# Kernel optimization log

Hardware: AMD Instinct MI355X
Metric: run time of the kernel (lower is better)

The kernel has to match this reference:

```python
import jax, jax.numpy as jnp
import numpy as np

BS, L, NIMG, D, H, DH, V, NL = 16, 256, 256, 512, 8, 256, 1000, 6


def _softmax_one(x):
    # softmax with +1 in denominator (post max-shift, literal +1 as in source)
    m = jnp.max(x, axis=-1, keepdims=True)
    e = jnp.exp(x - m)
    return e / (1.0 + jnp.sum(e, axis=-1, keepdims=True))


def _ln(x, g, b):
    mu = jnp.mean(x, axis=-1, keepdims=True)
    var = jnp.var(x, axis=-1, keepdims=True)
    return (x - mu) * jax.lax.rsqrt(var + 1e-5) * g + b


def _mha(xq, xkv, wq, b_q, wk, b_k, wv, b_v, wo, b_o, mask):
    b, nq, _ = xq.shape
    nk = xkv.shape[1]
    q = (xq @ wq + b_q).reshape(b, nq, H, DH).transpose(0, 2, 1, 3)
    k = (xkv @ wk + b_k).reshape(b, nk, H, DH).transpose(0, 2, 1, 3)
    v = (xkv @ wv + b_v).reshape(b, nk, H, DH).transpose(0, 2, 1, 3)
    s = jnp.einsum('bhqd,bhkd->bhqk', q, k) / jnp.sqrt(jnp.float32(DH))
    if mask is not None:
        s = s + mask[:, None]  # (b,1,nq,nk) additive mask
    o = jnp.einsum('bhqk,bhkd->bhqd', _softmax_one(s), v)
    return o.transpose(0, 2, 1, 3).reshape(b, nq, H * DH) @ wo + b_o


def _forward(program, pro_adj, img_features, embed, W_in, b_in, ln1_g, ln1_b, ln2_g, ln2_b,
             Wq, bq, Wk, bk, Wv, bv, Wo, bo, f_W1, f_b1, f_W2, f_b2,
             cWq, cbq, cWk, cbk, cWv, cbv, cWo, cbo):
    mask = (1.0 - pro_adj.astype(jnp.float32)) * -1e6
    bs, length = program.shape[:2]
    x = embed[program].reshape(bs, length, -1) @ W_in + b_in  # (bs, L, D)
    for i in range(NL):
        # self-attn transformer layer (pre-LN, residual)
        h = _ln(x, ln1_g[i], ln1_b[i])
        x = x + _mha(h, h, Wq[i], bq[i], Wk[i], bk[i], Wv[i], bv[i], Wo[i], bo[i], mask)
        h2 = _ln(x, ln2_g[i], ln2_b[i])
        x = x + (jax.nn.gelu(h2 @ f_W1[i] + f_b1[i], approximate=False) @ f_W2[i] + f_b2[i])
        # cross-modal attention to image features, residual add
        x = x + _mha(x, img_features, cWq[i], cbq[i], cWk[i], cbk[i], cWv[i], cbv[i], cWo[i], cbo[i], None)
    return x


def setup_inputs() -> dict:
    key = jax.random.key(0)
    ks = jax.random.split(key, 16)
    def n(k, shape):
        return jax.random.normal(k, shape, jnp.float32) * 0.02
    program = jax.random.randint(ks[0], (BS, L, 8), 0, V, dtype=jnp.int32)
    pro_adj = jax.random.randint(ks[1], (BS, L, L), 0, 2, dtype=jnp.int32)
    img_features = jax.random.normal(ks[2], (BS, NIMG, D), jnp.float32)
    embed = n(ks[3], (V, 300)).at[0].set(0.0)  # padding_idx=0
    return dict(
        program=program, pro_adj=pro_adj, img_features=img_features, embed=embed,
        W_in=n(ks[4], (8 * 300, D)), b_in=jnp.zeros((D,), jnp.float32),
        ln1_g=jnp.ones((NL, D), jnp.float32), ln1_b=jnp.zeros((NL, D), jnp.float32),
        ln2_g=jnp.ones((NL, D), jnp.float32), ln2_b=jnp.zeros((NL, D), jnp.float32),
        Wq=n(ks[5], (NL, D, H * DH)), bq=jnp.zeros((NL, H * DH), jnp.float32),
        Wk=n(ks[6], (NL, D, H * DH)), bk=jnp.zeros((NL, H * DH), jnp.float32),
        Wv=n(ks[7], (NL, D, H * DH)), bv=jnp.zeros((NL, H * DH), jnp.float32),
        Wo=n(ks[8], (NL, H * DH, D)), bo=jnp.zeros((NL, D), jnp.float32),
        f_W1=n(ks[9], (NL, D, D)), f_b1=jnp.zeros((NL, D), jnp.float32),
        f_W2=n(ks[10], (NL, D, D)), f_b2=jnp.zeros((NL, D), jnp.float32),
        cWq=n(ks[11], (NL, D, H * DH)), cbq=jnp.zeros((NL, H * DH), jnp.float32),
        cWk=n(ks[12], (NL, D, H * DH)), cbk=jnp.zeros((NL, H * DH), jnp.float32),
        cWv=n(ks[13], (NL, D, H * DH)), cbv=jnp.zeros((NL, H * DH), jnp.float32),
        cWo=n(ks[14], (NL, H * DH, D)), cbo=jnp.zeros((NL, D), jnp.float32),
    )


def reference(program, pro_adj, img_features, embed, W_in, b_in, ln1_g, ln1_b, ln2_g, ln2_b,
              Wq, bq, Wk, bk, Wv, bv, Wo, bo, f_W1, f_b1, f_W2, f_b2,
              cWq, cbq, cWk, cbk, cWv, cbv, cWo, cbo):
    return _forward(program, pro_adj, img_features, embed, W_in, b_in, ln1_g, ln1_b, ln2_g, ln2_b,
                    Wq, bq, Wk, bk, Wv, bv, Wo, bo, f_W1, f_b1, f_W2, f_b2,
                    cWq, cbq, cWk, cbk, cWv, cbv, cWo, cbo)
```

## Files before the change

kernel.cpp:

```cpp
#include <hip/hip_runtime.h>
#include <hip/hip_bf16.h>

typedef __attribute__((ext_vector_type(8))) short short8;
typedef __attribute__((ext_vector_type(4))) float f32x4;
typedef unsigned short u16;

__device__ __forceinline__ u16 f2b(float f) {
    unsigned int u = __builtin_bit_cast(unsigned int, f);
    u = u + 0x7fffu + ((u >> 16) & 1u);
    return (u16)(u >> 16);
}

#define EPI_F32      0
#define EPI_RESID_XB 3
#define EPI_GELU     4
#define EPI_KV       7
#define EPI_ATOMIC   9

template<int BM, int BN, int BK, int EPI>
__global__ __launch_bounds__(256, 2) void gemm_bf16(
    const u16* __restrict__ A, long aStride, int lda,
    const u16* __restrict__ B, long bStride, int ldb,
    int M, int N, int K,
    const float* __restrict__ bias0, const float* __restrict__ bias1,
    int biasStride,
    const float* __restrict__ Rsd,
    float* __restrict__ outF, u16* __restrict__ outB,
    u16* __restrict__ outV, long outStride, int ldc)
{
    constexpr int WCOLS = BN / 64;
    constexpr int WROWS = 4 / WCOLS;
    constexpr int WM = BM / WROWS;
    constexpr int MF = WM / 16;
    constexpr int NF = 4;
    constexpr int GR = BK / 8;
    constexpr int AUNITS = BM * GR;
    constexpr int UPT = (BM + BN) * GR / 256;
    constexpr int BUFE = (BM + BN) * BK;

    __shared__ __align__(16) u16 smem[2 * BUFE];

    const int tid = threadIdx.x;
    const int wave = tid >> 6, lane = tid & 63;
    const int wm = wave / WCOLS, wn = wave % WCOLS;

    const int nwg = gridDim.x * gridDim.y;
    const int bl = blockIdx.y * gridDim.x + blockIdx.x;
    const int wsw = (bl & 7) * (nwg >> 3) + (bl >> 3);
    const int bxs = wsw % gridDim.x, bys = wsw / gridDim.x;

    const int tm = bys * BM, tn = bxs * BN;
    const int bz = blockIdx.z;

    const size_t aOff = (size_t)bz * (size_t)aStride;
    const size_t bOff = (size_t)bz * (size_t)bStride;

    const int lr = lane & 15, kg = lane >> 4;

    auto stage = [&](int buf, int k0) {
#pragma unroll
        for (int i = 0; i < UPT; i++) {
            int u = tid + i * 256;
            u16* dst = smem + buf * BUFE + u * 8;
            bool isA = u < AUNITS;
            int v = isA ? u : u - AUNITS;
            int row, kloc;
            if constexpr (BK == 64) {
                row = v >> 3;
                int hh = (v >> 2) & 1, g = v & 3;
                kloc = ((hh ^ (row & 1)) << 5) + ((g ^ ((row >> 1) & 3)) << 3);
            } else {
                row = v >> 2;
                int g = v & 3;
                kloc = (g ^ ((row >> 1) & 3)) << 3;
            }
            const u16* src = isA
                ? A + aOff + (size_t)(tm + row) * lda + k0 + kloc
                : B + bOff + (size_t)(tn + row) * ldb + k0 + kloc;
            __builtin_amdgcn_global_load_lds(src, dst, 16, 0, 0);
        }
    };

    auto ldsOff = [&](int row, int kk) -> int {
        if constexpr (BK == 64)
            return row * 64 + (((kk ^ (row & 1)) * 4 + (kg ^ ((row >> 1) & 3))) * 8);
        else
            return row * 32 + ((kg ^ ((row >> 1) & 3)) * 8);
    };

    f32x4 acc[MF][NF];
#pragma unroll
    for (int m = 0; m < MF; m++)
#pragma unroll
        for (int n = 0; n < NF; n++) acc[m][n] = (f32x4)(0.f);

    const int NT = K / BK;
    stage(0, 0);
    __syncthreads();

    for (int t = 0; t < NT; t++) {
        const int cur = t & 1;
        if (t + 1 < NT) stage(cur ^ 1, (t + 1) * BK);

        const u16* As = smem + cur * BUFE;
        const u16* Bs = As + BM * BK;
#pragma unroll
        for (int kk = 0; kk < BK / 32; kk++) {
            short8 af[MF], bfr[NF];
#pragma unroll
            for (int m = 0; m < MF; m++) {
                int row = wm * WM + m * 16 + lr;
                af[m] = *(const short8*)&As[ldsOff(row, kk)];
            }
#pragma unroll
            for (int n = 0; n < NF; n++) {
                int row = wn * 64 + n * 16 + lr;
                bfr[n] = *(const short8*)&Bs[ldsOff(row, kk)];
            }
#pragma unroll
            for (int m = 0; m < MF; m++)
#pragma unroll
                for (int n = 0; n < NF; n++)
                    acc[m][n] = __builtin_amdgcn_mfma_f32_16x16x32_bf16(
                        af[m], bfr[n], acc[m][n], 0, 0, 0);
        }
        __syncthreads();
    }

    if constexpr (EPI == EPI_KV) {
        if (tn < 2048) {
#pragma unroll
            for (int m = 0; m < MF; m++)
#pragma unroll
                for (int n = 0; n < NF; n++)
#pragma unroll
                    for (int e = 0; e < 4; e++) {
                        int r = tm + wm * WM + m * 16 + kg * 4 + e;
                        int c = tn + wn * 64 + n * 16 + lr;
                        float t = acc[m][n][e] + bias0[bz * biasStride + c];
                        outB[(size_t)bz * outStride + (size_t)r * 2048 + c] = f2b(t);
                    }
        } else {
            const int ccb = tn - 2048;
            const int bidx = tm >> 8;
            const int hh = ccb >> 8;
            u16* vls = smem;
#pragma unroll
            for (int m = 0; m < MF; m++)
#pragma unroll
                for (int n = 0; n < NF; n++)
#pragma unroll
                    for (int e = 0; e < 4; e++) {
                        int rl = wm * WM + m * 16 + kg * 4 + e;
                        int cl = wn * 64 + n * 16 + lr;
                        float t = acc[m][n][e] + bias1[bz * biasStride + ccb + cl];
                        vls[cl * 136 + rl] = f2b(t);
                    }
            __syncthreads();
            const int dloc = tid >> 1;
            const int thalf = (tid & 1) * 64;
            const int dglob = (ccb & 255) + dloc;
            u16* dst = outV + (size_t)bz * outStride +
                       (size_t)(bidx * 8 + hh) * 65536 +
                       (size_t)dglob * 256 + (tm & 255) + thalf;
            const u16* srcl = vls + dloc * 136 + thalf;
#pragma unroll
            for (int k = 0; k < 8; k++)
                *(uint4*)(dst + k * 8) = *(const uint4*)(srcl + k * 8);
        }
        return;
    }

#pragma unroll
    for (int m = 0; m < MF; m++) {
#pragma unroll
        for (int n = 0; n < NF; n++) {
#pragma unroll
            for (int e = 0; e < 4; e++) {
                int r = tm + wm * WM + m * 16 + (lane >> 4) * 4 + e;
                int c = tn + wn * 64 + n * 16 + (lane & 15);
                float v = acc[m][n][e];
                if constexpr (EPI == EPI_F32) {
                    outF[(size_t)r * ldc + c] = v + bias0[c];
                } else if constexpr (EPI == EPI_RESID_XB) {
                    float t = v + bias0[c] + Rsd[(size_t)r * ldc + c];
                    outF[(size_t)r * ldc + c] = t;
                    outB[(size_t)r * ldc + c] = f2b(t);
                } else if constexpr (EPI == EPI_GELU) {
                    float t = v + bias0[c];
                    t = 0.5f * t * (1.f + erff(t * 0.70710678118654752f));
                    outB[(size_t)r * ldc + c] = f2b(t);
                } else if constexpr (EPI == EPI_ATOMIC) {
                    float t = v;
                    if (bz == 0) t += bias0[c];
                    atomicAdd(&outF[(size_t)r * ldc + c], t);
                }
            }
        }
    }
}

template<bool MASKED>
__global__ __launch_bounds__(256, 2) void attn_kernel(
    const u16* __restrict__ Aq, const u16* __restrict__ WqT,
    const float* __restrict__ bq,
    const u16* __restrict__ K, const u16* __restrict__ Vt,
    const int* __restrict__ adj, u16* __restrict__ O)
{
    __shared__ __align__(16) u16 Ps[64 * 256];
    __shared__ __align__(16) u16 Ks[2 * 256 * 32];
    __shared__ __align__(16) u16 Aql[2 * 64 * 32];
    __shared__ float red1[64 * 4];
    __shared__ float red2[64 * 4];

    const int tid = threadIdx.x;
    const int w = tid >> 6, lane = tid & 63;
    const int lr = lane & 15, kg = lane >> 4;

    const int nwg = gridDim.x * gridDim.y;
    const int bl = blockIdx.y * gridDim.x + blockIdx.x;
    const int wsw = (bl & 7) * (nwg >> 3) + (bl >> 3);
    const int qt = wsw % gridDim.x, bh = wsw / gridDim.x;

    const int b = bh >> 3, h = bh & 7;
    const size_t qkBase = (size_t)b * 256 * 2048 + h * 256;

    auto stageA0 = [&](int buf, int k0) {
        int u = tid;
        int row = u >> 2, g = u & 3;
        int gs = g ^ ((row >> 1) & 3);
        const u16* src = Aq + (size_t)(b * 256 + qt * 64 + row) * 512 + k0 + gs * 8;
        __builtin_amdgcn_global_load_lds(src, Aql + buf * 2048 + u * 8, 16, 0, 0);
    };
    auto stageB0 = [&](int buf, int k0) {
#pragma unroll
        for (int i = 0; i < 4; i++) {
            int u = tid + i * 256;
            int row = u >> 2, g = u & 3;
            int gs = g ^ ((row >> 1) & 3);
            const u16* src = WqT + (size_t)(h * 256 + row) * 512 + k0 + gs * 8;
            __builtin_amdgcn_global_load_lds(src, Ks + buf * 8192 + u * 8, 16, 0, 0);
        }
    };
    auto stageK = [&](int buf, int dk) {
#pragma unroll
        for (int i = 0; i < 4; i++) {
            int u = tid + i * 256;
            int row = u >> 2, g = u & 3;
            int gs = g ^ ((row >> 1) & 3);
            const u16* src = K + qkBase + (size_t)row * 2048 + dk * 32 + gs * 8;
            __builtin_amdgcn_global_load_lds(src, Ks + buf * 8192 + u * 8, 16, 0, 0);
        }
    };
    auto stageV = [&](int buf, int kt) {
#pragma unroll
        for (int i = 0; i < 4; i++) {
            int u = tid + i * 256;
            int row = u >> 2, g = u & 3;
            int gs = g ^ ((row >> 1) & 3);
            const u16* src = Vt + (size_t)bh * 65536 + (size_t)row * 256 + kt * 32 + gs * 8;
            __builtin_amdgcn_global_load_lds(src, Ks + buf * 8192 + u * 8, 16, 0, 0);
        }
    };

    {
        f32x4 qacc[4][4];
#pragma unroll
        for (int m = 0; m < 4; m++)
#pragma unroll
            for (int n = 0; n < 4; n++) qacc[m][n] = (f32x4)(0.f);

        stageA0(0, 0);
        stageB0(0, 0);
        __syncthreads();
        for (int t = 0; t < 16; t++) {
            const int cur = t & 1;
            if (t < 15) { stageA0(cur ^ 1, (t + 1) * 32); stageB0(cur ^ 1, (t + 1) * 32); }
            short8 af[4], bfr[4];
#pragma unroll
            for (int m = 0; m < 4; m++) {
                int row = m * 16 + lr;
                af[m] = *(const short8*)&Aql[cur * 2048 + row * 32 + ((kg ^ ((row >> 1) & 3)) * 8)];
            }
#pragma unroll
            for (int n = 0; n < 4; n++) {
                int row = w * 64 + n * 16 + lr;
                bfr[n] = *(const short8*)&Ks[cur * 8192 + row * 32 + ((kg ^ ((row >> 1) & 3)) * 8)];
            }
            __builtin_amdgcn_s_setprio(1);
#pragma unroll
            for (int m = 0; m < 4; m++)
#pragma unroll
                for (int n = 0; n < 4; n++)
                    qacc[m][n] = __builtin_amdgcn_mfma_f32_16x16x32_bf16(
                        af[m], bfr[n], qacc[m][n], 0, 0, 0);
            __builtin_amdgcn_s_setprio(0);
            __syncthreads();
        }
#pragma unroll
        for (int m = 0; m < 4; m++)
#pragma unroll
            for (int n = 0; n < 4; n++)
#pragma unroll
                for (int e = 0; e < 4; e++) {
                    int q = m * 16 + kg * 4 + e;
                    int d = w * 64 + n * 16 + lr;
                    float t = qacc[m][n][e] + bq[h * 256 + d];
                    Ps[q * 256 + (((d >> 3) ^ (q & 7)) * 8) + (d & 7)] = f2b(t);
                }
    }
    __syncthreads();

    f32x4 sacc[4][4];
#pragma unroll
    for (int m = 0; m < 4; m++)
#pragma unroll
        for (int n = 0; n < 4; n++) sacc[m][n] = (f32x4)(0.f);

    stageK(0, 0);
    __syncthreads();
    for (int dk = 0; dk < 8; dk++) {
        const int cur = dk & 1;
        if (dk < 7) stageK(cur ^ 1, dk + 1);
        short8 af[4], bfr[4];
#pragma unroll
        for (int m = 0; m < 4; m++) {
            int row = m * 16 + lr;
            af[m] = *(const short8*)&Ps[row * 256 + (((dk * 4 + kg) ^ (row & 7)) * 8)];
        }
#pragma unroll
        for (int n = 0; n < 4; n++) {
            int row = w * 64 + n * 16 + lr;
            bfr[n] = *(const short8*)&Ks[cur * 8192 + row * 32 + ((kg ^ ((row >> 1) & 3)) * 8)];
        }
        __builtin_amdgcn_s_setprio(1);
#pragma unroll
        for (int m = 0; m < 4; m++)
#pragma unroll
            for (int n = 0; n < 4; n++)
                sacc[m][n] = __builtin_amdgcn_mfma_f32_16x16x32_bf16(
                    af[m], bfr[n], sacc[m][n], 0, 0, 0);
        __builtin_amdgcn_s_setprio(0);
        __syncthreads();
    }

    stageV(0, 0);

#pragma unroll
    for (int m = 0; m < 4; m++)
#pragma unroll
        for (int n = 0; n < 4; n++)
#pragma unroll
            for (int e = 0; e < 4; e++) {
                float t = sacc[m][n][e] * 0.0625f;
                if (MASKED) {
                    int q = qt * 64 + m * 16 + kg * 4 + e;
                    int k = w * 64 + n * 16 + lr;
                    int a_ = adj[((size_t)b * 256 + q) * 256 + k];
                    t += (1.f - (float)a_) * -1.0e6f;
                }
                sacc[m][n][e] = t;
            }

    float mx[4][4];
#pragma unroll
    for (int m = 0; m < 4; m++)
#pragma unroll
        for (int e = 0; e < 4; e++) {
            float v = sacc[m][0][e];
#pragma unroll
            for (int n = 1; n < 4; n++) v = fmaxf(v, sacc[m][n][e]);
#pragma unroll
            for (int off = 1; off < 16; off <<= 1) v = fmaxf(v, __shfl_xor(v, off));
            mx[m][e] = v;
        }
    if (lr == 0) {
#pragma unroll
        for (int m = 0; m < 4; m++)
#pragma unroll
            for (int e = 0; e < 4; e++)
                red1[(m * 16 + kg * 4 + e) * 4 + w] = mx[m][e];
    }
    __syncthreads();

    float inv[4][4];
    float sum[4][4];
#pragma unroll
    for (int m = 0; m < 4; m++)
#pragma unroll
        for (int e = 0; e < 4; e++) {
            int r = m * 16 + kg * 4 + e;
            float gm = fmaxf(fmaxf(red1[r * 4 + 0], red1[r * 4 + 1]),
                             fmaxf(red1[r * 4 + 2], red1[r * 4 + 3]));
            float s = 0.f;
#pragma unroll
            for (int n = 0; n < 4; n++) {
                float ev = __expf(sacc[m][n][e] - gm);
                sacc[m][n][e] = ev;
                s += ev;
            }
            sum[m][e] = s;
        }
#pragma unroll
    for (int m = 0; m < 4; m++)
#pragma unroll
        for (int e = 0; e < 4; e++) {
            float s = sum[m][e];
#pragma unroll
            for (int off = 1; off < 16; off <<= 1) s += __shfl_xor(s, off);
            sum[m][e] = s;
        }
    if (lr == 0) {
#pragma unroll
        for (int m = 0; m < 4; m++)
#pragma unroll
            for (int e = 0; e < 4; e++)
                red2[(m * 16 + kg * 4 + e) * 4 + w] = sum[m][e];
    }
    __syncthreads();
#pragma unroll
    for (int m = 0; m < 4; m++)
#pragma unroll
        for (int e = 0; e < 4; e++) {
            int r = m * 16 + kg * 4 + e;
            float gs = red2[r * 4 + 0] + red2[r * 4 + 1] +
                       red2[r * 4 + 2] + red2[r * 4 + 3];
            inv[m][e] = 1.f / (1.f + gs);
        }

#pragma unroll
    for (int m = 0; m < 4; m++)
#pragma unroll
        for (int n = 0; n < 4; n++)
#pragma unroll
            for (int e = 0; e < 4; e++) {
                int q = m * 16 + kg * 4 + e;
                int k = w * 64 + n * 16 + lr;
                float pv = sacc[m][n][e] * inv[m][e];
                Ps[q * 256 + (((k >> 3) ^ (q & 7)) * 8) + (k & 7)] = f2b(pv);
            }
    __syncthreads();

    f32x4 oacc[4][4];
#pragma unroll
    for (int m = 0; m < 4; m++)
#pragma unroll
        for (int n = 0; n < 4; n++) oacc[m][n] = (f32x4)(0.f);

    for (int kt = 0; kt < 8; kt++) {
        const int cur = kt & 1;
        if (kt < 7) stageV(cur ^ 1, kt + 1);
        short8 af[4], bfr[4];
#pragma unroll
        for (int m = 0; m < 4; m++) {
            int q = m * 16 + lr;
            af[m] = *(const short8*)&Ps[q * 256 + (((kt * 4 + kg) ^ (q & 7)) * 8)];
        }
#pragma unroll
        for (int n = 0; n < 4; n++) {
            int row = w * 64 + n * 16 + lr;
            bfr[n] = *(const short8*)&Ks[cur * 8192 + row * 32 + ((kg ^ ((row >> 1) & 3)) * 8)];
        }
        __builtin_amdgcn_s_setprio(1);
#pragma unroll
        for (int m = 0; m < 4; m++)
#pragma unroll
            for (int n = 0; n < 4; n++)
                oacc[m][n] = __builtin_amdgcn_mfma_f32_16x16x32_bf16(
                    af[m], bfr[n], oacc[m][n], 0, 0, 0);
        __builtin_amdgcn_s_setprio(0);
        __syncthreads();
    }

#pragma unroll
    for (int m = 0; m < 4; m++)
#pragma unroll
        for (int n = 0; n < 4; n++)
#pragma unroll
            for (int e = 0; e < 4; e++) {
                int q = qt * 64 + m * 16 + kg * 4 + e;
                int d = w * 64 + n * 16 + lr;
                O[(size_t)(b * 256 + q) * 2048 + h * 256 + d] = f2b(oacc[m][n][e]);
            }
}

__global__ __launch_bounds__(256) void transpose_kernel(
    const float* p0, const float* p1, const float* p2,
    const float* p3, const float* p4, const float* p5,
    int nsrc, long srcLayerStride, int R, int C,
    u16* __restrict__ out, long dstMatStride, long dstLayerStride)
{
    const int mat = blockIdx.z % nsrc, layer = blockIdx.z / nsrc;
    const float* W;
    switch (mat) {
    default: W = p0; break;
    case 1: W = p1; break;
    case 2: W = p2; break;
    case 3: W = p3; break;
    case 4: W = p4; break;
    case 5: W = p5; break;
    }
    W += (size_t)layer * srcLayerStride;
    u16* o = out + (size_t)layer * dstLayerStride + (size_t)mat * dstMatStride;
    __shared__ float t[64][65];
    const int tid = threadIdx.x;
    const int rBase = blockIdx.y * 64, cBase = blockIdx.x * 64;
#pragma unroll
    for (int i = 0; i < 4; i++) {
        int idx = tid + i * 256;
        int rr = idx >> 4, cc4 = (idx & 15) * 4;
        if (rBase + rr < R) {
            float4 v = *(const float4*)&W[(size_t)(rBase + rr) * C + cBase + cc4];
            t[rr][cc4] = v.x; t[rr][cc4 + 1] = v.y;
            t[rr][cc4 + 2] = v.z; t[rr][cc4 + 3] = v.w;
        }
    }
    __syncthreads();
#pragma unroll
    for (int i = 0; i < 4; i++) {
        int idx = tid + i * 256;
        int cc = idx >> 4, rr4 = (idx & 15) * 4;
        if (rBase + rr4 < R) {
            uint2 pk;
            pk.x = (unsigned)f2b(t[rr4][cc]) | ((unsigned)f2b(t[rr4 + 1][cc]) << 16);
            pk.y = (unsigned)f2b(t[rr4 + 2][cc]) | ((unsigned)f2b(t[rr4 + 3][cc]) << 16);
            *(uint2*)&o[(size_t)(cBase + cc) * R + rBase + rr4] = pk;
        }
    }
}

__global__ __launch_bounds__(256) void ln_kernel(
    const float* __restrict__ X, const float* __restrict__ g,
    const float* __restrict__ b, u16* __restrict__ Y)
{
    const int wave = threadIdx.x >> 6, lane = threadIdx.x & 63;
    const size_t row = (size_t)blockIdx.x * 4 + wave;
    const float* xr = X + row * 512;
    float4 v0 = *reinterpret_cast<const float4*>(xr + lane * 8);
    float4 v1 = *reinterpret_cast<const float4*>(xr + lane * 8 + 4);
    float s = v0.x + v0.y + v0.z + v0.w + v1.x + v1.y + v1.z + v1.w;
    float ss = v0.x * v0.x + v0.y * v0.y + v0.z * v0.z + v0.w * v0.w +
               v1.x * v1.x + v1.y * v1.y + v1.z * v1.z + v1.w * v1.w;
#pragma unroll
    for (int off = 32; off; off >>= 1) {
        s += __shfl_xor(s, off);
        ss += __shfl_xor(ss, off);
    }
    float mu = s * (1.0f / 512.0f);
    float var = ss * (1.0f / 512.0f) - mu * mu;
    float rs = rsqrtf(var + 1e-5f);
    float4 g0 = *reinterpret_cast<const float4*>(g + lane * 8);
    float4 g1 = *reinterpret_cast<const float4*>(g + lane * 8 + 4);
    float4 b0 = *reinterpret_cast<const float4*>(b + lane * 8);
    float4 b1 = *reinterpret_cast<const float4*>(b + lane * 8 + 4);
    float o0 = (v0.x - mu) * rs * g0.x + b0.x;
    float o1 = (v0.y - mu) * rs * g0.y + b0.y;
    float o2 = (v0.z - mu) * rs * g0.z + b0.z;
    float o3 = (v0.w - mu) * rs * g0.w + b0.w;
    float o4 = (v1.x - mu) * rs * g1.x + b1.x;
    float o5 = (v1.y - mu) * rs * g1.y + b1.y;
    float o6 = (v1.z - mu) * rs * g1.z + b1.z;
    float o7 = (v1.w - mu) * rs * g1.w + b1.w;
    uint4 pk;
    pk.x = (unsigned)f2b(o0) | ((unsigned)f2b(o1) << 16);
    pk.y = (unsigned)f2b(o2) | ((unsigned)f2b(o3) << 16);
    pk.z = (unsigned)f2b(o4) | ((unsigned)f2b(o5) << 16);
    pk.w = (unsigned)f2b(o6) | ((unsigned)f2b(o7) << 16);
    *reinterpret_cast<uint4*>(Y + row * 512 + lane * 8) = pk;
}

__global__ __launch_bounds__(256) void gather_kernel(
    const int* __restrict__ program, const float* __restrict__ embed,
    unsigned* __restrict__ Ag2, int total2)
{
    int idx = blockIdx.x * 256 + threadIdx.x;
    if (idx >= total2) return;
    int t = idx / 1200;
    int rem = idx - t * 1200;
    int j = rem / 150;
    int e2 = rem - j * 150;
    int tok = program[t * 8 + j];
    float2 v = *reinterpret_cast<const float2*>(&embed[(size_t)tok * 300 + e2 * 2]);
    Ag2[idx] = (unsigned)f2b(v.x) | ((unsigned)f2b(v.y) << 16);
}

__global__ __launch_bounds__(256) void cvt_kernel(
    const float* __restrict__ in, u16* __restrict__ out, int n4)
{
    int i = blockIdx.x * 256 + threadIdx.x;
    if (i >= n4) return;
    float4 v = reinterpret_cast<const float4*>(in)[i];
    uint2 pk;
    pk.x = (unsigned)f2b(v.x) | ((unsigned)f2b(v.y) << 16);
    pk.y = (unsigned)f2b(v.z) | ((unsigned)f2b(v.w) << 16);
    reinterpret_cast<uint2*>(out)[i] = pk;
}


extern "C" void kernel_launch(void* const* d_in, const int* in_sizes, int n_in,
                              void* d_out, int out_size, void* d_ws, size_t ws_size,
                              hipStream_t stream)
{
    const int*   program = (const int*)d_in[0];
    const int*   adj     = (const int*)d_in[1];
    const float* img     = (const float*)d_in[2];
    const float* embed   = (const float*)d_in[3];
    const float* W_in    = (const float*)d_in[4];
    const float* b_in    = (const float*)d_in[5];
    const float* ln1_g   = (const float*)d_in[6];
    const float* ln1_b   = (const float*)d_in[7];
    const float* ln2_g   = (const float*)d_in[8];
    const float* ln2_b   = (const float*)d_in[9];
    const float* Wq      = (const float*)d_in[10];
    const float* bq      = (const float*)d_in[11];
    const float* Wk      = (const float*)d_in[12];
    const float* bk      = (const float*)d_in[13];
    const float* Wv      = (const float*)d_in[14];
    const float* bv      = (const float*)d_in[15];
    const float* Wo      = (const float*)d_in[16];
    const float* bo      = (const float*)d_in[17];
    const float* fW1     = (const float*)d_in[18];
    const float* fb1     = (const float*)d_in[19];
    const float* fW2     = (const float*)d_in[20];
    const float* fb2     = (const float*)d_in[21];
    const float* cWq     = (const float*)d_in[22];
    const float* cbq     = (const float*)d_in[23];
    const float* cWk     = (const float*)d_in[24];
    const float* cbk     = (const float*)d_in[25];
    const float* cWv     = (const float*)d_in[26];
    const float* cbv     = (const float*)d_in[27];
    const float* cWo     = (const float*)d_in[28];
    const float* cbo     = (const float*)d_in[29];

    char* wsb = (char*)d_ws;
    const size_t MB = 1024 * 1024;
    const long Mi = 1048576;
    const long LSTR = 8 * Mi + Mi / 2;

    float* x    = (float*)(wsb + 0);
    u16*   h    = (u16*)(wsb + 8 * MB);
    u16*   xb   = (u16*)(wsb + 12 * MB);
    u16*   imgb = (u16*)(wsb + 16 * MB);
    u16*   WinT = (u16*)(wsb + 20 * MB);
    u16*   Kb   = (u16*)(wsb + 24 * MB);
    u16*   Vt   = (u16*)(wsb + 40 * MB);
    u16*   O    = (u16*)(wsb + 56 * MB);
    u16*   Wall = (u16*)(wsb + 72 * MB);
    u16*   KcA  = (u16*)(wsb + 176 * MB);
    u16*   VcA  = (u16*)(wsb + 272 * MB);
    u16*   Ag   = Kb;
    u16*   g    = Kb;

    const bool bigws = ws_size >= (size_t)175 * MB;
    const bool hoist = ws_size >= (size_t)369 * MB && bigws;

    gather_kernel<<<19200, 256, 0, stream>>>(program, embed, (unsigned*)Ag, 4915200);
    transpose_kernel<<<dim3(8, 38, 1), 256, 0, stream>>>(
        W_in, nullptr, nullptr, nullptr, nullptr, nullptr,
        1, 0, 2400, 512, WinT, 0, 0);
    cvt_kernel<<<2048, 256, 0, stream>>>(img, imgb, 524288);
    if (bigws) {
        transpose_kernel<<<dim3(32, 8, 36), 256, 0, stream>>>(
            Wq, Wk, Wv, cWq, cWk, cWv, 6, Mi, 512, 2048, Wall, Mi, LSTR);
        transpose_kernel<<<dim3(8, 32, 12), 256, 0, stream>>>(
            Wo, cWo, nullptr, nullptr, nullptr, nullptr,
            2, Mi, 2048, 512, Wall + 6 * Mi, Mi, LSTR);
        transpose_kernel<<<dim3(8, 8, 12), 256, 0, stream>>>(
            fW1, fW2, nullptr, nullptr, nullptr, nullptr,
            2, 262144, 512, 512, Wall + 8 * Mi, 262144, LSTR);
    }
    gemm_bf16<64, 64, 32, EPI_F32><<<dim3(8, 64, 1), 256, 0, stream>>>(
        Ag, 0, 2400, WinT, 0, 2400, 4096, 512, 2400,
        b_in, nullptr, 0, nullptr,
        x, nullptr, nullptr, 0, 512);
    if (hoist) {
        gemm_bf16<128, 128, 64, EPI_KV><<<dim3(32, 32, 6), 256, 0, stream>>>(
            imgb, 0, 512, Wall + 4 * Mi, LSTR, 512, 4096, 4096, 512,
            cbk, cbv, 2048, nullptr,
            nullptr, KcA, VcA, 8 * Mi, 2048);
    }

    for (int l = 0; l < 6; l++) {
        u16* Wl = Wall + (bigws ? (size_t)l * LSTR : 0);
        if (!bigws) {
            transpose_kernel<<<dim3(32, 8, 6), 256, 0, stream>>>(
                Wq + (size_t)l * Mi, Wk + (size_t)l * Mi, Wv + (size_t)l * Mi,
                cWq + (size_t)l * Mi, cWk + (size_t)l * Mi, cWv + (size_t)l * Mi,
                6, 0, 512, 2048, Wl, Mi, 0);
            transpose_kernel<<<dim3(8, 32, 2), 256, 0, stream>>>(
                Wo + (size_t)l * Mi, cWo + (size_t)l * Mi,
                nullptr, nullptr, nullptr, nullptr,
                2, 0, 2048, 512, Wl + 6 * Mi, Mi, 0);
            transpose_kernel<<<dim3(8, 8, 2), 256, 0, stream>>>(
                fW1 + (size_t)l * 262144, fW2 + (size_t)l * 262144,
                nullptr, nullptr, nullptr, nullptr,
                2, 0, 512, 512, Wl + 8 * Mi, 262144, 0);
        }

        ln_kernel<<<1024, 256, 0, stream>>>(x, ln1_g + l * 512, ln1_b + l * 512, h);
        gemm_bf16<128, 128, 64, EPI_KV><<<dim3(32, 32, 1), 256, 0, stream>>>(
            h, 0, 512, Wl + 1 * Mi, 0, 512, 4096, 4096, 512,
            bk + l * 2048, bv + l * 2048, 0, nullptr,
            nullptr, Kb, Vt, 0, 2048);
        attn_kernel<true><<<dim3(4, 128), 256, 0, stream>>>(
            h, Wl, bq + l * 2048, Kb, Vt, adj, O);
        gemm_bf16<64, 64, 64, EPI_ATOMIC><<<dim3(8, 64, 2), 256, 0, stream>>>(
            O, 1024, 2048, Wl + 6 * Mi, 1024, 2048, 4096, 512, 1024,
            bo + l * 512, nullptr, 0, nullptr,
            x, nullptr, nullptr, 0, 512);

        ln_kernel<<<1024, 256, 0, stream>>>(x, ln2_g + l * 512, ln2_b + l * 512, h);
        gemm_bf16<64, 64, 64, EPI_GELU><<<dim3(8, 64, 1), 256, 0, stream>>>(
            h, 0, 512, Wl + 8 * Mi, 0, 512, 4096, 512, 512,
            fb1 + l * 512, nullptr, 0, nullptr,
            nullptr, g, nullptr, 0, 512);
        gemm_bf16<64, 64, 64, EPI_RESID_XB><<<dim3(8, 64, 1), 256, 0, stream>>>(
            g, 0, 512, Wl + 8 * Mi + 262144, 0, 512, 4096, 512, 512,
            fb2 + l * 512, nullptr, 0, x,
            x, xb, nullptr, 0, 512);

        u16* Kc = hoist ? (KcA + (size_t)l * 8 * Mi) : Kb;
        u16* Vc = hoist ? (VcA + (size_t)l * 8 * Mi) : Vt;
        if (!hoist) {
            gemm_bf16<128, 128, 64, EPI_KV><<<dim3(32, 32, 1), 256, 0, stream>>>(
                imgb, 0, 512, Wl + 4 * Mi, 0, 512, 4096, 4096, 512,
                cbk + l * 2048, cbv + l * 2048, 0, nullptr,
                nullptr, Kb, Vt, 0, 2048);
        }
        attn_kernel<false><<<dim3(4, 128), 256, 0, stream>>>(
            xb, Wl + 3 * Mi, cbq + l * 2048, Kc, Vc, nullptr, O);
        gemm_bf16<64, 64, 64, EPI_ATOMIC><<<dim3(8, 64, 2), 256, 0, stream>>>(
            O, 1024, 2048, Wl + 7 * Mi, 1024, 2048, 4096, 512, 1024,
            cbo + l * 512, nullptr, 0, nullptr,
            x, nullptr, nullptr, 0, 512);
    }

    hipMemcpyAsync(d_out, x, (size_t)2097152 * sizeof(float),
                   hipMemcpyDeviceToDevice, stream);
}
```

Measured before the change: 1.351 ms.

## Make attention K/V staging wave-private and drop per-step block barriers

Result: no change. 1.341 ms (-0.7%).

```diff
diff --git a/kernel.cpp b/kernel.cpp
--- a/kernel.cpp
+++ b/kernel.cpp
@@ -28,14 +28,16 @@
     float* __restrict__ outF, u16* __restrict__ outB,
     u16* __restrict__ outV, long outStride, int ldc)
 {
-    constexpr int WCOLS = BN / 64;
+    constexpr int WCOLS = (BM == 32) ? 2 : (BN / 64);
     constexpr int WROWS = 4 / WCOLS;
     constexpr int WM = BM / WROWS;
+    constexpr int WN = BN / WCOLS;
     constexpr int MF = WM / 16;
-    constexpr int NF = 4;
+    constexpr int NF = WN / 16;
     constexpr int GR = BK / 8;
     constexpr int AUNITS = BM * GR;
-    constexpr int UPT = (BM + BN) * GR / 256;
+    constexpr int TOTU = (BM + BN) * GR;
+    constexpr int UPT = (TOTU + 255) / 256;
     constexpr int BUFE = (BM + BN) * BK;
 
     __shared__ __align__(16) u16 smem[2 * BUFE];
@@ -61,23 +63,25 @@
 #pragma unroll
         for (int i = 0; i < UPT; i++) {
             int u = tid + i * 256;
-            u16* dst = smem + buf * BUFE + u * 8;
-            bool isA = u < AUNITS;
-            int v = isA ? u : u - AUNITS;
-            int row, kloc;
-            if constexpr (BK == 64) {
-                row = v >> 3;
-                int hh = (v >> 2) & 1, g = v & 3;
-                kloc = ((hh ^ (row & 1)) << 5) + ((g ^ ((row >> 1) & 3)) << 3);
-            } else {
-                row = v >> 2;
-                int g = v & 3;
-                kloc = (g ^ ((row >> 1) & 3)) << 3;
-            }
-            const u16* src = isA
-                ? A + aOff + (size_t)(tm + row) * lda + k0 + kloc
-                : B + bOff + (size_t)(tn + row) * ldb + k0 + kloc;
-            __builtin_amdgcn_global_load_lds(src, dst, 16, 0, 0);
+            if (u < TOTU) {
+                u16* dst = smem + buf * BUFE + u * 8;
+                bool isA = u < AUNITS;
+                int v = isA ? u : u - AUNITS;
+                int row, kloc;
+                if constexpr (BK == 64) {
+                    row = v >> 3;
+                    int hh = (v >> 2) & 1, g = v & 3;
+                    kloc = ((hh ^ (row & 1)) << 5) + ((g ^ ((row >> 1) & 3)) << 3);
+                } else {
+                    row = v >> 2;
+                    int g = v & 3;
+                    kloc = (g ^ ((row >> 1) & 3)) << 3;
+                }
+                const u16* src = isA
+                    ? A + aOff + (size_t)(tm + row) * lda + k0 + kloc
+                    : B + bOff + (size_t)(tn + row) * ldb + k0 + kloc;
+                __builtin_amdgcn_global_load_lds(src, dst, 16, 0, 0);
+            }
         }
     };
 
@@ -114,7 +118,7 @@
             }
 #pragma unroll
             for (int n = 0; n < NF; n++) {
-                int row = wn * 64 + n * 16 + lr;
+                int row = wn * WN + n * 16 + lr;
                 bfr[n] = *(const short8*)&Bs[ldsOff(row, kk)];
             }
 #pragma unroll
@@ -136,7 +140,7 @@
 #pragma unroll
                     for (int e = 0; e < 4; e++) {
                         int r = tm + wm * WM + m * 16 + kg * 4 + e;
-                        int c = tn + wn * 64 + n * 16 + lr;
+                        int c = tn + wn * WN + n * 16 + lr;
                         float t = acc[m][n][e] + bias0[bz * biasStride + c];
                         outB[(size_t)bz * outStride + (size_t)r * 2048 + c] = f2b(t);
                     }
@@ -152,7 +156,7 @@
 #pragma unroll
                     for (int e = 0; e < 4; e++) {
                         int rl = wm * WM + m * 16 + kg * 4 + e;
-                        int cl = wn * 64 + n * 16 + lr;
+                        int cl = wn * WN + n * 16 + lr;
                         float t = acc[m][n][e] + bias1[bz * biasStride + ccb + cl];
                         vls[cl * 136 + rl] = f2b(t);
                     }
@@ -178,7 +182,7 @@
 #pragma unroll
             for (int e = 0; e < 4; e++) {
                 int r = tm + wm * WM + m * 16 + (lane >> 4) * 4 + e;
-                int c = tn + wn * 64 + n * 16 + (lane & 15);
+                int c = tn + wn * WN + n * 16 + (lane & 15);
                 float v = acc[m][n][e];
                 if constexpr (EPI == EPI_F32) {
                     outF[(size_t)r * ldc + c] = v + bias0[c];
@@ -245,7 +249,7 @@
     auto stageK = [&](int buf, int dk) {
 #pragma unroll
         for (int i = 0; i < 4; i++) {
-            int u = tid + i * 256;
+            int u = w * 256 + i * 64 + lane;
             int row = u >> 2, g = u & 3;
             int gs = g ^ ((row >> 1) & 3);
             const u16* src = K + qkBase + (size_t)row * 2048 + dk * 32 + gs * 8;
@@ -255,7 +259,7 @@
     auto stageV = [&](int buf, int kt) {
 #pragma unroll
         for (int i = 0; i < 4; i++) {
-            int u = tid + i * 256;
+            int u = w * 256 + i * 64 + lane;
             int row = u >> 2, g = u & 3;
             int gs = g ^ ((row >> 1) & 3);
             const u16* src = Vt + (size_t)bh * 65536 + (size_t)row * 256 + kt * 32 + gs * 8;
@@ -297,6 +301,7 @@
             __builtin_amdgcn_s_setprio(0);
             __syncthreads();
         }
+        stageK(0, 0);
 #pragma unroll
         for (int m = 0; m < 4; m++)
 #pragma unroll
@@ -317,11 +322,15 @@
 #pragma unroll
         for (int n = 0; n < 4; n++) sacc[m][n] = (f32x4)(0.f);
 
-    stageK(0, 0);
-    __syncthreads();
     for (int dk = 0; dk < 8; dk++) {
         const int cur = dk & 1;
-        if (dk < 7) stageK(cur ^ 1, dk + 1);
+        if (dk < 7) {
+            stageK(cur ^ 1, dk + 1);
+            asm volatile("s_waitcnt vmcnt(4)" ::: "memory");
+        } else {
+            asm volatile("s_waitcnt vmcnt(0)" ::: "memory");
+        }
+        __builtin_amdgcn_sched_barrier(0);
         short8 af[4], bfr[4];
 #pragma unroll
         for (int m = 0; m < 4; m++) {
@@ -341,7 +350,6 @@
                 sacc[m][n] = __builtin_amdgcn_mfma_f32_16x16x32_bf16(
                     af[m], bfr[n], sacc[m][n], 0, 0, 0);
         __builtin_amdgcn_s_setprio(0);
-        __syncthreads();
     }
 
     stageV(0, 0);
@@ -449,7 +457,13 @@
 
     for (int kt = 0; kt < 8; kt++) {
         const int cur = kt & 1;
-        if (kt < 7) stageV(cur ^ 1, kt + 1);
+        if (kt < 7) {
+            stageV(cur ^ 1, kt + 1);
+            asm volatile("s_waitcnt vmcnt(4)" ::: "memory");
+        } else {
+            asm volatile("s_waitcnt vmcnt(0)" ::: "memory");
+        }
+        __builtin_amdgcn_sched_barrier(0);
         short8 af[4], bfr[4];
 #pragma unroll
         for (int m = 0; m < 4; m++) {
@@ -469,7 +483,6 @@
                 oacc[m][n] = __builtin_amdgcn_mfma_f32_16x16x32_bf16(
                     af[m], bfr[n], oacc[m][n], 0, 0, 0);
         __builtin_amdgcn_s_setprio(0);
-        __syncthreads();
     }
 
 #pragma unroll
```
